# Kernel tuning notes

Measured on AMD Instinct MI355X. Metric: run time of the kernel, lower is better.

Reference implementation:

```python
import jax, jax.numpy as jnp
import numpy as np

N_NODES = 100000
N_EDGES = 1600000
D_IN, D_HID, D_OUT = 64, 64, 40


def _init_linear(key, out_c, in_c, bias=True):
    # PyTorch nn.Linear default init: U(-1/sqrt(in), 1/sqrt(in))
    bound = 1.0 / np.sqrt(in_c)
    kw, kb = jax.random.split(key)
    W = jax.random.uniform(kw, (out_c, in_c), jnp.float32, -bound, bound)
    if bias:
        b = jax.random.uniform(kb, (out_c,), jnp.float32, -bound, bound)
        return W, b
    return W


def setup_inputs() -> dict:
    key = jax.random.key(0)
    ks = jax.random.split(key, 8)
    x = jax.random.normal(ks[0], (N_NODES, D_IN), jnp.float32)
    edge_index = jax.random.randint(ks[1], (2, N_EDGES), 0, N_NODES, jnp.int64)
    W1l, b1 = _init_linear(ks[2], D_HID, D_IN, bias=True)   # lin_l (aggregated msgs)
    W1r = _init_linear(ks[3], D_HID, D_IN, bias=False)      # lin_r (root/self)
    W2l, b2 = _init_linear(ks[4], D_OUT, D_HID, bias=True)
    W2r = _init_linear(ks[5], D_OUT, D_HID, bias=False)
    return {"x": x, "edge_index": edge_index,
            "W1l": W1l, "b1": b1, "W1r": W1r,
            "W2l": W2l, "b2": b2, "W2r": W2r}


def _sage_conv(x, src, dst, Wl, bl, Wr):
    # mean aggregation of source-node features onto destination nodes
    msgs = x[src]                                            # [E, d] gather
    agg = jax.ops.segment_sum(msgs, dst, num_segments=N_NODES)
    deg = jax.ops.segment_sum(jnp.ones((src.shape[0],), x.dtype), dst,
                              num_segments=N_NODES)
    mean = agg / jnp.maximum(deg, 1.0)[:, None]              # [N, d]
    # out = lin_l(mean) + lin_r(x)
    return mean @ Wl.T + bl + x @ Wr.T


def reference(x, edge_index, W1l, b1, W1r, W2l, b2, W2r):
    src, dst = edge_index[0], edge_index[1]
    h = _sage_conv(x, src, dst, W1l, b1, W1r)
    h = jax.nn.relu(h)
    # dropout is identity in inference mode
    h = _sage_conv(h, src, dst, W2l, b2, W2r)
    return jax.nn.log_softmax(h, axis=1)
```

## Files before the change

kernel.cpp:

```cpp
#include <hip/hip_runtime.h>
#include <math.h>

#define N_NODES 100000
#define N_EDGES 1600000
#define D 64
#define DOUT 40
#define NBUCK ((N_NODES + 255) / 256)
#define CHUNK 4096
#define NCHUNK ((N_EDGES + CHUNK - 1) / CHUNK)
#define PTHREADS 512
#define BCAP 4864

typedef __attribute__((ext_vector_type(8))) short bf16x8v;
typedef __attribute__((ext_vector_type(4))) float f32x4v;

__device__ inline float bf2f(unsigned u) {
  union { unsigned i; float f; } v;
  v.i = u << 16;
  return v.f;
}
__device__ inline unsigned f2bf(float f) {
  union { float f; unsigned i; } v;
  v.f = f;
  unsigned r = v.i + 0x7fffu + ((v.i >> 16) & 1u);
  return r >> 16;
}
__device__ inline void addpk(float2& a, unsigned u) {
  union { unsigned i; float f; } lo, hi;
  lo.i = u << 16;
  hi.i = u & 0xffff0000u;
  a.x += lo.f;
  a.y += hi.f;
}
__device__ inline void addrow4(float2* A, uint4 r) {
  addpk(A[0], r.x); addpk(A[1], r.y); addpk(A[2], r.z); addpk(A[3], r.w);
}

__global__ __launch_bounds__(PTHREADS) void prep_kernel(
    const float* __restrict__ x, unsigned short* __restrict__ xbf,
    const float* __restrict__ W1l, const float* __restrict__ W1r,
    const float* __restrict__ W2l, const float* __restrict__ W2r,
    const float* __restrict__ b2, unsigned short* __restrict__ Wcat1,
    unsigned short* __restrict__ Wcat2, float* __restrict__ b2p,
    const int* __restrict__ src, const int* __restrict__ dst,
    int* __restrict__ bcnt, unsigned* __restrict__ binned) {
  __shared__ unsigned ent[CHUNK];
  __shared__ unsigned short sbk[CHUNK];
  __shared__ int cnt[512], scn[512], pos[512], base[512];
  int t = threadIdx.x;
  int blk = blockIdx.x;
  int gtid = blk * PTHREADS + t;
  int nth = NCHUNK * PTHREADS;

  const int n8 = N_NODES * D / 8;
  for (int i = gtid; i < n8; i += nth) {
    const float4* p = reinterpret_cast<const float4*>(x) + (size_t)i * 2;
    float4 a = p[0], b = p[1];
    uint4 o;
    o.x = f2bf(a.x) | (f2bf(a.y) << 16);
    o.y = f2bf(a.z) | (f2bf(a.w) << 16);
    o.z = f2bf(b.x) | (f2bf(b.y) << 16);
    o.w = f2bf(b.z) | (f2bf(b.w) << 16);
    reinterpret_cast<uint4*>(xbf)[i] = o;
  }
  const int NW = 64 * 128 + 48 * 128 + 48;
  for (int i = gtid; i < NW; i += nth) {
    if (i < 64 * 128) {
      int o = i >> 7, k = i & 127;
      float v = (k < 64) ? W1l[o * 64 + k] : W1r[o * 64 + (k - 64)];
      Wcat1[i] = (unsigned short)f2bf(v);
    } else if (i < 64 * 128 + 48 * 128) {
      int j = i - 64 * 128;
      int o = j >> 7, k = j & 127;
      float v = (o < DOUT) ? ((k < 64) ? W2l[o * 64 + k] : W2r[o * 64 + (k - 64)]) : 0.0f;
      Wcat2[j] = (unsigned short)f2bf(v);
    } else {
      int j = i - 64 * 128 - 48 * 128;
      b2p[j] = (j < DOUT) ? b2[j] : 0.0f;
    }
  }
  cnt[t] = 0;
  __syncthreads();
  int cbase = blk * CHUNK;
  int cc = min(CHUNK, N_EDGES - cbase);
  unsigned my_e[8];
  int my_b[8];
  int nmine = 0;
#pragma unroll
  for (int i = 0; i < 8; ++i) {
    int li = t + i * PTHREADS;
    if (li < cc) {
      int s = src[cbase + li];
      int d = dst[cbase + li];
      int b = d >> 8;
      my_e[nmine] = ((unsigned)(d & 255) << 24) | (unsigned)s;
      my_b[nmine] = b;
      nmine++;
      atomicAdd(&cnt[b], 1);
    }
  }
  __syncthreads();
  scn[t] = cnt[t];
  __syncthreads();
  for (int off = 1; off < 512; off <<= 1) {
    int v = (t >= off) ? scn[t - off] : 0;
    __syncthreads();
    scn[t] += v;
    __syncthreads();
  }
  pos[t] = scn[t] - cnt[t];
  __syncthreads();
  for (int i = 0; i < nmine; ++i) {
    int slot = atomicAdd(&pos[my_b[i]], 1);
    ent[slot] = my_e[i];
    sbk[slot] = (unsigned short)my_b[i];
  }
  __syncthreads();
  for (int b = t; b < NBUCK; b += PTHREADS)
    if (cnt[b] > 0) base[b] = atomicAdd(&bcnt[b], cnt[b]);
  __syncthreads();
  for (int i = t; i < cc; i += PTHREADS) {
    int b = sbk[i];
    int excl = scn[b] - cnt[b];
    binned[(size_t)b * BCAP + base[b] + (i - excl)] = ent[i];
  }
}

__global__ __launch_bounds__(512) void fine_kernel(
    const unsigned* __restrict__ binned, const int* __restrict__ bcnt,
    int* __restrict__ rs, int* __restrict__ re_, int* __restrict__ csr, int N) {
  __shared__ unsigned ent[BCAP];
  __shared__ int c[256], p[256], pos[256];
  int b = blockIdx.x;
  int t = threadIdx.x;
  int cc = bcnt[b];
  int s0 = b * BCAP;
  if (t < 256) c[t] = 0;
  __syncthreads();
  for (int i = t; i < cc; i += 512) {
    unsigned u = binned[s0 + i];
    ent[i] = u;
    atomicAdd(&c[u >> 24], 1);
  }
  __syncthreads();
  if (t < 256) p[t] = c[t];
  __syncthreads();
  for (int off = 1; off < 256; off <<= 1) {
    int v = 0;
    if (t < 256 && t >= off) v = p[t - off];
    __syncthreads();
    if (t < 256) p[t] += v;
    __syncthreads();
  }
  if (t < 256) {
    int excl = p[t] - c[t];
    int node = b * 256 + t;
    if (node < N) {
      rs[node] = s0 + excl;
      re_[node] = s0 + excl + c[t];
    }
    pos[t] = excl;
  }
  __syncthreads();
  for (int i = t; i < cc; i += 512) {
    unsigned u = ent[i];
    int slot = atomicAdd(&pos[u >> 24], 1);
    csr[s0 + slot] = (int)(u & 0xFFFFFFu);
  }
}

__global__ __launch_bounds__(256) void agg_kernel(
    const unsigned short* __restrict__ feat, const int* __restrict__ rs,
    const int* __restrict__ re_, const int* __restrict__ csr,
    unsigned short* __restrict__ msbf, int N) {
  int wv = (blockIdx.x * 256 + threadIdx.x) >> 6;
  int n0 = wv * 2;
  if (n0 >= N) return;
  int n1 = n0 + 1;
  int lane = threadIdx.x & 63;
  int g = lane >> 3;
  int t = lane & 7;
  int s0 = rs[n0], en0 = re_[n0];
  int s1 = rs[n1], en1 = re_[n1];
  float2 A[4] = {{0.f,0.f},{0.f,0.f},{0.f,0.f},{0.f,0.f}};
  float2 B[4] = {{0.f,0.f},{0.f,0.f},{0.f,0.f},{0.f,0.f}};
  int e0 = s0 + g, e1 = s1 + g;

  {
    bool v0a = e0 < en0, v0b = e0 + 8 < en0;
    bool v1a = e1 < en1, v1b = e1 + 8 < en1;
    int q0a = min(e0, max(en0 - 1, 0));
    int q0b = min(e0 + 8, max(en0 - 1, 0));
    int q1a = min(e1, max(en1 - 1, 0));
    int q1b = min(e1 + 8, max(en1 - 1, 0));
    int i0a = min(csr[q0a], N - 1);
    int i0b = min(csr[q0b], N - 1);
    int i1a = min(csr[q1a], N - 1);
    int i1b = min(csr[q1b], N - 1);
    uint4 r0a = *reinterpret_cast<const uint4*>(feat + (size_t)i0a * D + t * 8);
    uint4 r0b = *reinterpret_cast<const uint4*>(feat + (size_t)i0b * D + t * 8);
    uint4 r1a = *reinterpret_cast<const uint4*>(feat + (size_t)i1a * D + t * 8);
    uint4 r1b = *reinterpret_cast<const uint4*>(feat + (size_t)i1b * D + t * 8);
    if (v0a) addrow4(A, r0a);
    if (v0b) addrow4(A, r0b);
    if (v1a) addrow4(B, r1a);
    if (v1b) addrow4(B, r1b);
    e0 += 16;
    e1 += 16;
  }
  for (; e0 + 8 < en0; e0 += 16) {
    int i0 = csr[e0];
    int i1 = csr[e0 + 8];
    uint4 r0 = *reinterpret_cast<const uint4*>(feat + (size_t)i0 * D + t * 8);
    uint4 r1 = *reinterpret_cast<const uint4*>(feat + (size_t)i1 * D + t * 8);
    addrow4(A, r0);
    addrow4(A, r1);
  }
  if (e0 < en0) {
    int i0 = csr[e0];
    uint4 r0 = *reinterpret_cast<const uint4*>(feat + (size_t)i0 * D + t * 8);
    addrow4(A, r0);
  }
  for (; e1 + 8 < en1; e1 += 16) {
    int i0 = csr[e1];
    int i1 = csr[e1 + 8];
    uint4 r0 = *reinterpret_cast<const uint4*>(feat + (size_t)i0 * D + t * 8);
    uint4 r1 = *reinterpret_cast<const uint4*>(feat + (size_t)i1 * D + t * 8);
    addrow4(B, r0);
    addrow4(B, r1);
  }
  if (e1 < en1) {
    int i0 = csr[e1];
    uint4 r0 = *reinterpret_cast<const uint4*>(feat + (size_t)i0 * D + t * 8);
    addrow4(B, r0);
  }
#pragma unroll
  for (int j = 0; j < 4; ++j) {
    A[j].x += __shfl_xor(A[j].x, 8, 64);  A[j].y += __shfl_xor(A[j].y, 8, 64);
    A[j].x += __shfl_xor(A[j].x, 16, 64); A[j].y += __shfl_xor(A[j].y, 16, 64);
    A[j].x += __shfl_xor(A[j].x, 32, 64); A[j].y += __shfl_xor(A[j].y, 32, 64);
    B[j].x += __shfl_xor(B[j].x, 8, 64);  B[j].y += __shfl_xor(B[j].y, 8, 64);
    B[j].x += __shfl_xor(B[j].x, 16, 64); B[j].y += __shfl_xor(B[j].y, 16, 64);
    B[j].x += __shfl_xor(B[j].x, 32, 64); B[j].y += __shfl_xor(B[j].y, 32, 64);
  }
  float inv0 = 1.0f / fmaxf((float)(en0 - s0), 1.0f);
  float inv1 = 1.0f / fmaxf((float)(en1 - s1), 1.0f);
  float va[8] = {A[0].x, A[0].y, A[1].x, A[1].y, A[2].x, A[2].y, A[3].x, A[3].y};
  float vb[8] = {B[0].x, B[0].y, B[1].x, B[1].y, B[2].x, B[2].y, B[3].x, B[3].y};
  float ma = va[0], mb = vb[0];
#pragma unroll
  for (int j = 1; j < 8; ++j) {
    if (g == j) { ma = va[j]; mb = vb[j]; }
  }
  msbf[(size_t)n0 * D + t * 8 + g] = (unsigned short)f2bf(ma * inv0);
  msbf[(size_t)n1 * D + t * 8 + g] = (unsigned short)f2bf(mb * inv1);
}

__global__ __launch_bounds__(256) void lin1_kernel(
    const unsigned short* __restrict__ xbf, const unsigned short* __restrict__ msbf,
    const unsigned short* __restrict__ Wcat, const float* __restrict__ b1,
    unsigned short* __restrict__ hbf, int N) {
  int wid = (blockIdx.x * 256 + threadIdx.x) >> 6;
  int ntiles = N >> 4;
  if (wid >= ntiles) return;
  int lane = threadIdx.x & 63;
  int col = lane & 15;
  int k0 = (lane >> 4) * 8;
  int base = wid * 16;
  const unsigned short* am = msbf + (size_t)(base + col) * D;
  const unsigned short* ax = xbf + (size_t)(base + col) * D;
  bf16x8v a0 = *(const bf16x8v*)(am + k0);
  bf16x8v a1 = *(const bf16x8v*)(am + 32 + k0);
  bf16x8v a2 = *(const bf16x8v*)(ax + k0);
  bf16x8v a3 = *(const bf16x8v*)(ax + 32 + k0);
  f32x4v acc0 = {0.f, 0.f, 0.f, 0.f}, acc1 = acc0, acc2 = acc0, acc3 = acc0;
#define LIN1_CT(CT, ACC)                                                      \
  {                                                                           \
    const unsigned short* w = Wcat + ((CT)*16 + col) * 128 + k0;              \
    bf16x8v b0 = *(const bf16x8v*)(w);                                        \
    bf16x8v b1v = *(const bf16x8v*)(w + 32);                                  \
    bf16x8v b2v = *(const bf16x8v*)(w + 64);                                  \
    bf16x8v b3v = *(const bf16x8v*)(w + 96);                                  \
    ACC = __builtin_amdgcn_mfma_f32_16x16x32_bf16(a0, b0, ACC, 0, 0, 0);      \
    ACC = __builtin_amdgcn_mfma_f32_16x16x32_bf16(a1, b1v, ACC, 0, 0, 0);     \
    ACC = __builtin_amdgcn_mfma_f32_16x16x32_bf16(a2, b2v, ACC, 0, 0, 0);     \
    ACC = __builtin_amdgcn_mfma_f32_16x16x32_bf16(a3, b3v, ACC, 0, 0, 0);     \
  }
  LIN1_CT(0, acc0) LIN1_CT(1, acc1) LIN1_CT(2, acc2) LIN1_CT(3, acc3)
#undef LIN1_CT
  int rbase = (lane >> 4) * 4;
  float bias0 = b1[col], bias1 = b1[16 + col], bias2 = b1[32 + col], bias3 = b1[48 + col];
#pragma unroll
  for (int r = 0; r < 4; ++r) {
    size_t rowoff = (size_t)(base + rbase + r) * D;
    hbf[rowoff + col]      = (unsigned short)f2bf(fmaxf(acc0[r] + bias0, 0.f));
    hbf[rowoff + 16 + col] = (unsigned short)f2bf(fmaxf(acc1[r] + bias1, 0.f));
    hbf[rowoff + 32 + col] = (unsigned short)f2bf(fmaxf(acc2[r] + bias2, 0.f));
    hbf[rowoff + 48 + col] = (unsigned short)f2bf(fmaxf(acc3[r] + bias3, 0.f));
  }
}

__global__ __launch_bounds__(256) void lin2_kernel(
    const unsigned short* __restrict__ hbf, const unsigned short* __restrict__ msbf,
    const unsigned short* __restrict__ Wcat, const float* __restrict__ b2p,
    float* __restrict__ out, int N) {
  int wid = (blockIdx.x * 256 + threadIdx.x) >> 6;
  int ntiles = N >> 4;
  if (wid >= ntiles) return;
  int lane = threadIdx.x & 63;
  int col = lane & 15;
  int k0 = (lane >> 4) * 8;
  int base = wid * 16;
  const unsigned short* am = msbf + (size_t)(base + col) * D;
  const unsigned short* ah = hbf + (size_t)(base + col) * D;
  bf16x8v a0 = *(const bf16x8v*)(am + k0);
  bf16x8v a1 = *(const bf16x8v*)(am + 32 + k0);
  bf16x8v a2 = *(const bf16x8v*)(ah + k0);
  bf16x8v a3 = *(const bf16x8v*)(ah + 32 + k0);
  f32x4v acc0 = {0.f, 0.f, 0.f, 0.f}, acc1 = acc0, acc2 = acc0;
#define LIN2_CT(CT, ACC)                                                      \
  {                                                                           \
    const unsigned short* w = Wcat + ((CT)*16 + col) * 128 + k0;              \
    bf16x8v b0 = *(const bf16x8v*)(w);                                        \
    bf16x8v b1v = *(const bf16x8v*)(w + 32);                                  \
    bf16x8v b2v = *(const bf16x8v*)(w + 64);                                  \
    bf16x8v b3v = *(const bf16x8v*)(w + 96);                                  \
    ACC = __builtin_amdgcn_mfma_f32_16x16x32_bf16(a0, b0, ACC, 0, 0, 0);      \
    ACC = __builtin_amdgcn_mfma_f32_16x16x32_bf16(a1, b1v, ACC, 0, 0, 0);     \
    ACC = __builtin_amdgcn_mfma_f32_16x16x32_bf16(a2, b2v, ACC, 0, 0, 0);     \
    ACC = __builtin_amdgcn_mfma_f32_16x16x32_bf16(a3, b3v, ACC, 0, 0, 0);     \
  }
  LIN2_CT(0, acc0) LIN2_CT(1, acc1) LIN2_CT(2, acc2)
#undef LIN2_CT
  int rbase = (lane >> 4) * 4;
  float bias0 = b2p[col], bias1 = b2p[16 + col], bias2 = b2p[32 + col];
  bool v2ok = (col < 8);
#pragma unroll
  for (int r = 0; r < 4; ++r) {
    float v0 = acc0[r] + bias0;
    float v1 = acc1[r] + bias1;
    float v2 = v2ok ? (acc2[r] + bias2) : -INFINITY;
    float mx = fmaxf(fmaxf(v0, v1), v2);
    mx = fmaxf(mx, __shfl_xor(mx, 1, 64));
    mx = fmaxf(mx, __shfl_xor(mx, 2, 64));
    mx = fmaxf(mx, __shfl_xor(mx, 4, 64));
    mx = fmaxf(mx, __shfl_xor(mx, 8, 64));
    float sm = expf(v0 - mx) + expf(v1 - mx) + (v2ok ? expf(v2 - mx) : 0.f);
    sm += __shfl_xor(sm, 1, 64);
    sm += __shfl_xor(sm, 2, 64);
    sm += __shfl_xor(sm, 4, 64);
    sm += __shfl_xor(sm, 8, 64);
    float ls = mx + logf(sm);
    size_t rowoff = (size_t)(base + rbase + r) * DOUT;
    out[rowoff + col] = v0 - ls;
    out[rowoff + 16 + col] = v1 - ls;
    if (v2ok) out[rowoff + 32 + col] = v2 - ls;
  }
}

extern "C" void kernel_launch(void* const* d_in, const int* in_sizes, int n_in,
                              void* d_out, int out_size, void* d_ws, size_t ws_size,
                              hipStream_t stream) {
  const float* x   = (const float*)d_in[0];
  const int*   ei  = (const int*)d_in[1];
  const float* W1l = (const float*)d_in[2];
  const float* b1  = (const float*)d_in[3];
  const float* W1r = (const float*)d_in[4];
  const float* W2l = (const float*)d_in[5];
  const float* b2  = (const float*)d_in[6];
  const float* W2r = (const float*)d_in[7];
  float* out = (float*)d_out;

  const int* src = ei;
  const int* dst = ei + N_EDGES;

  char* ws = (char*)d_ws;
  size_t featB = (size_t)N_NODES * D * sizeof(unsigned short);
  unsigned short* xbf = (unsigned short*)ws;
  unsigned short* hbf = (unsigned short*)(ws + featB);
  int* csr  = (int*)(ws + 2 * featB);
  int* rs   = csr + (size_t)NBUCK * BCAP;
  int* re_  = rs + N_NODES;
  int* bcnt = re_ + N_NODES;
  char* scratch = (char*)(bcnt + NBUCK);
  scratch = (char*)(((uintptr_t)scratch + 15) & ~(uintptr_t)15);
  unsigned* binned     = (unsigned*)scratch;
  unsigned short* ms1  = (unsigned short*)scratch;
  unsigned short* ms2  = xbf;
  unsigned short* Wcat1 = (unsigned short*)(scratch + featB);
  unsigned short* Wcat2 = Wcat1 + 64 * 128;
  float* b2p            = (float*)(Wcat2 + 48 * 128);

  const int AGG_BLOCKS = (N_NODES + 7) / 8;
  const int LIN_BLOCKS = ((N_NODES / 16) + 3) / 4;

  hipMemsetAsync(bcnt, 0, NBUCK * sizeof(int), stream);
  prep_kernel<<<NCHUNK, PTHREADS, 0, stream>>>(x, xbf, W1l, W1r, W2l, W2r, b2,
                                               Wcat1, Wcat2, b2p, src, dst, bcnt, binned);
  fine_kernel<<<NBUCK, 512, 0, stream>>>(binned, bcnt, rs, re_, csr, N_NODES);

  agg_kernel<<<AGG_BLOCKS, 256, 0, stream>>>(xbf, rs, re_, csr, ms1, N_NODES);
  lin1_kernel<<<LIN_BLOCKS, 256, 0, stream>>>(xbf, ms1, Wcat1, b1, hbf, N_NODES);

  agg_kernel<<<AGG_BLOCKS, 256, 0, stream>>>(hbf, rs, re_, csr, ms2, N_NODES);
  lin2_kernel<<<LIN_BLOCKS, 256, 0, stream>>>(hbf, ms2, Wcat2, b2p, out, N_NODES);
}
```

Baseline: 147.1 us.

## Fuse neighbor aggregation with linear layers via shared-memory tiles

Merges the agg and lin kernels of each SAGE layer into one kernel. Each 512-thread block aggregates 16 nodes, eight waves doing two nodes each, and writes the bf16 means into LDS. After a barrier, one wave runs the MFMA linear layer and the epilogue. This removes the global round-trip for the mean features and two kernel launches. In exchange, seven of eight waves sit idle during the matmul phase, and the block-level barrier ties the MFMA work to the slowest gather wave.

```diff
diff --git a/kernel.cpp b/kernel.cpp
--- a/kernel.cpp
+++ b/kernel.cpp
@@ -169,23 +169,16 @@
   }
 }
 
-__global__ __launch_bounds__(256) void agg_kernel(
-    const unsigned short* __restrict__ feat, const int* __restrict__ rs,
-    const int* __restrict__ re_, const int* __restrict__ csr,
-    unsigned short* __restrict__ msbf, int N) {
-  int wv = (blockIdx.x * 256 + threadIdx.x) >> 6;
-  int n0 = wv * 2;
-  if (n0 >= N) return;
+__device__ inline void agg2(const unsigned short* __restrict__ feat,
+                            const int* __restrict__ rs, const int* __restrict__ re_,
+                            const int* __restrict__ csr, int n0, int N,
+                            int g, int t, float& ma, float& mb) {
   int n1 = n0 + 1;
-  int lane = threadIdx.x & 63;
-  int g = lane >> 3;
-  int t = lane & 7;
   int s0 = rs[n0], en0 = re_[n0];
   int s1 = rs[n1], en1 = re_[n1];
   float2 A[4] = {{0.f,0.f},{0.f,0.f},{0.f,0.f},{0.f,0.f}};
   float2 B[4] = {{0.f,0.f},{0.f,0.f},{0.f,0.f},{0.f,0.f}};
   int e0 = s0 + g, e1 = s1 + g;
-
   {
     bool v0a = e0 < en0, v0b = e0 + 8 < en0;
     bool v1a = e1 < en1, v1b = e1 + 8 < en1;
@@ -247,114 +240,130 @@
   float inv1 = 1.0f / fmaxf((float)(en1 - s1), 1.0f);
   float va[8] = {A[0].x, A[0].y, A[1].x, A[1].y, A[2].x, A[2].y, A[3].x, A[3].y};
   float vb[8] = {B[0].x, B[0].y, B[1].x, B[1].y, B[2].x, B[2].y, B[3].x, B[3].y};
-  float ma = va[0], mb = vb[0];
+  ma = va[0]; mb = vb[0];
 #pragma unroll
   for (int j = 1; j < 8; ++j) {
     if (g == j) { ma = va[j]; mb = vb[j]; }
   }
-  msbf[(size_t)n0 * D + t * 8 + g] = (unsigned short)f2bf(ma * inv0);
-  msbf[(size_t)n1 * D + t * 8 + g] = (unsigned short)f2bf(mb * inv1);
-}
-
-__global__ __launch_bounds__(256) void lin1_kernel(
-    const unsigned short* __restrict__ xbf, const unsigned short* __restrict__ msbf,
+  ma *= inv0;
+  mb *= inv1;
+}
+
+__global__ __launch_bounds__(512) void fused1_kernel(
+    const unsigned short* __restrict__ xbf, const int* __restrict__ rs,
+    const int* __restrict__ re_, const int* __restrict__ csr,
     const unsigned short* __restrict__ Wcat, const float* __restrict__ b1,
     unsigned short* __restrict__ hbf, int N) {
-  int wid = (blockIdx.x * 256 + threadIdx.x) >> 6;
-  int ntiles = N >> 4;
-  if (wid >= ntiles) return;
+  __shared__ unsigned short msL[16][64];
+  int w = threadIdx.x >> 6;
   int lane = threadIdx.x & 63;
-  int col = lane & 15;
-  int k0 = (lane >> 4) * 8;
-  int base = wid * 16;
-  const unsigned short* am = msbf + (size_t)(base + col) * D;
-  const unsigned short* ax = xbf + (size_t)(base + col) * D;
-  bf16x8v a0 = *(const bf16x8v*)(am + k0);
-  bf16x8v a1 = *(const bf16x8v*)(am + 32 + k0);
-  bf16x8v a2 = *(const bf16x8v*)(ax + k0);
-  bf16x8v a3 = *(const bf16x8v*)(ax + 32 + k0);
-  f32x4v acc0 = {0.f, 0.f, 0.f, 0.f}, acc1 = acc0, acc2 = acc0, acc3 = acc0;
+  int g = lane >> 3;
+  int t = lane & 7;
+  int base = blockIdx.x * 16;
+  float ma, mb;
+  agg2(xbf, rs, re_, csr, base + w * 2, N, g, t, ma, mb);
+  msL[w * 2][t * 8 + g] = (unsigned short)f2bf(ma);
+  msL[w * 2 + 1][t * 8 + g] = (unsigned short)f2bf(mb);
+  __syncthreads();
+  if (threadIdx.x < 64) {
+    int col = lane & 15;
+    int k0 = (lane >> 4) * 8;
+    bf16x8v a0 = *(const bf16x8v*)(&msL[col][k0]);
+    bf16x8v a1 = *(const bf16x8v*)(&msL[col][32 + k0]);
+    const unsigned short* ax = xbf + (size_t)(base + col) * D;
+    bf16x8v a2 = *(const bf16x8v*)(ax + k0);
+    bf16x8v a3 = *(const bf16x8v*)(ax + 32 + k0);
+    f32x4v acc0 = {0.f, 0.f, 0.f, 0.f}, acc1 = acc0, acc2 = acc0, acc3 = acc0;
 #define LIN1_CT(CT, ACC)                                                      \
-  {                                                                           \
-    const unsigned short* w = Wcat + ((CT)*16 + col) * 128 + k0;              \
-    bf16x8v b0 = *(const bf16x8v*)(w);                                        \
-    bf16x8v b1v = *(const bf16x8v*)(w + 32);                                  \
-    bf16x8v b2v = *(const bf16x8v*)(w + 64);                                  \
-    bf16x8v b3v = *(const bf16x8v*)(w + 96);                                  \
-    ACC = __builtin_amdgcn_mfma_f32_16x16x32_bf16(a0, b0, ACC, 0, 0, 0);      \
-    ACC = __builtin_amdgcn_mfma_f32_16x16x32_bf16(a1, b1v, ACC, 0, 0, 0);     \
-    ACC = __builtin_amdgcn_mfma_f32_16x16x32_bf16(a2, b2v, ACC, 0, 0, 0);     \
-    ACC = __builtin_amdgcn_mfma_f32_16x16x32_bf16(a3, b3v, ACC, 0, 0, 0);     \
-  }
-  LIN1_CT(0, acc0) LIN1_CT(1, acc1) LIN1_CT(2, acc2) LIN1_CT(3, acc3)
+    {                                                                         \
+      const unsigned short* wp = Wcat + ((CT)*16 + col) * 128 + k0;           \
+      bf16x8v b0 = *(const bf16x8v*)(wp);                                     \
+      bf16x8v b1v = *(const bf16x8v*)(wp + 32);                               \
+      bf16x8v b2v = *(const bf16x8v*)(wp + 64);                               \
+      bf16x8v b3v = *(const bf16x8v*)(wp + 96);                               \
+      ACC = __builtin_amdgcn_mfma_f32_16x16x32_bf16(a0, b0, ACC, 0, 0, 0);    \
+      ACC = __builtin_amdgcn_mfma_f32_16x16x32_bf16(a1, b1v, ACC, 0, 0, 0);   \
+      ACC = __builtin_amdgcn_mfma_f32_16x16x32_bf16(a2, b2v, ACC, 0, 0, 0);   \
+      ACC = __builtin_amdgcn_mfma_f32_16x16x32_bf16(a3, b3v, ACC, 0, 0, 0);   \
+    }
+    LIN1_CT(0, acc0) LIN1_CT(1, acc1) LIN1_CT(2, acc2) LIN1_CT(3, acc3)
 #undef LIN1_CT
-  int rbase = (lane >> 4) * 4;
-  float bias0 = b1[col], bias1 = b1[16 + col], bias2 = b1[32 + col], bias3 = b1[48 + col];
+    int rbase = (lane >> 4) * 4;
+    float bias0 = b1[col], bias1 = b1[16 + col], bias2 = b1[32 + col], bias3 = b1[48 + col];
 #pragma unroll
-  for (int r = 0; r < 4; ++r) {
-    size_t rowoff = (size_t)(base + rbase + r) * D;
-    hbf[rowoff + col]      = (unsigned short)f2bf(fmaxf(acc0[r] + bias0, 0.f));
-    hbf[rowoff + 16 + col] = (unsigned short)f2bf(fmaxf(acc1[r] + bias1, 0.f));
-    hbf[rowoff + 32 + col] = (unsigned short)f2bf(fmaxf(acc2[r] + bias2, 0.f));
-    hbf[rowoff + 48 + col] = (unsigned short)f2bf(fmaxf(acc3[r] + bias3, 0.f));
-  }
-}
-
-__global__ __launch_bounds__(256) void lin2_kernel(
-    const unsigned short* __restrict__ hbf, const unsigned short* __restrict__ msbf,
+    for (int r = 0; r < 4; ++r) {
+      size_t rowoff = (size_t)(base + rbase + r) * D;
+      hbf[rowoff + col]      = (unsigned short)f2bf(fmaxf(acc0[r] + bias0, 0.f));
+      hbf[rowoff + 16 + col] = (unsigned short)f2bf(fmaxf(acc1[r] + bias1, 0.f));
+      hbf[rowoff + 32 + col] = (unsigned short)f2bf(fmaxf(acc2[r] + bias2, 0.f));
+      hbf[rowoff + 48 + col] = (unsigned short)f2bf(fmaxf(acc3[r] + bias3, 0.f));
+    }
+  }
+}
+
+__global__ __launch_bounds__(512) void fused2_kernel(
+    const unsigned short* __restrict__ hbf, const int* __restrict__ rs,
+    const int* __restrict__ re_, const int* __restrict__ csr,
     const unsigned short* __restrict__ Wcat, const float* __restrict__ b2p,
     float* __restrict__ out, int N) {
-  int wid = (blockIdx.x * 256 + threadIdx.x) >> 6;
-  int ntiles = N >> 4;
-  if (wid >= ntiles) return;
+  __shared__ unsigned short msL[16][64];
+  int w = threadIdx.x >> 6;
   int lane = threadIdx.x & 63;
-  int col = lane & 15;
-  int k0 = (lane >> 4) * 8;
-  int base = wid * 16;
-  const unsigned short* am = msbf + (size_t)(base + col) * D;
-  const unsigned short* ah = hbf + (size_t)(base + col) * D;
-  bf16x8v a0 = *(const bf16x8v*)(am + k0);
-  bf16x8v a1 = *(const bf16x8v*)(am + 32 + k0);
-  bf16x8v a2 = *(const bf16x8v*)(ah + k0);
-  bf16x8v a3 = *(const bf16x8v*)(ah + 32 + k0);
-  f32x4v acc0 = {0.f, 0.f, 0.f, 0.f}, acc1 = acc0, acc2 = acc0;
+  int g = lane >> 3;
+  int t = lane & 7;
+  int base = blockIdx.x * 16;
+  float ma, mb;
+  agg2(hbf, rs, re_, csr, base + w * 2, N, g, t, ma, mb);
+  msL[w * 2][t * 8 + g] = (unsigned short)f2bf(ma);
+  msL[w * 2 + 1][t * 8 + g] = (unsigned short)f2bf(mb);
+  __syncthreads();
+  if (threadIdx.x < 64) {
+    int col = lane & 15;
+    int k0 = (lane >> 4) * 8;
+    bf16x8v a0 = *(const bf16x8v*)(&msL[col][k0]);
+    bf16x8v a1 = *(const bf16x8v*)(&msL[col][32 + k0]);
+    const unsigned short* ah = hbf + (size_t)(base + col) * D;
+    bf16x8v a2 = *(const bf16x8v*)(ah + k0);
+    bf16x8v a3 = *(const bf16x8v*)(ah + 32 + k0);
+    f32x4v acc0 = {0.f, 0.f, 0.f, 0.f}, acc1 = acc0, acc2 = acc0;
 #define LIN2_CT(CT, ACC)                                                      \
-  {                                                                           \
-    const unsigned short* w = Wcat + ((CT)*16 + col) * 128 + k0;              \
-    bf16x8v b0 = *(const bf16x8v*)(w);                                        \
-    bf16x8v b1v = *(const bf16x8v*)(w + 32);                                  \
-    bf16x8v b2v = *(const bf16x8v*)(w + 64);                                  \
-    bf16x8v b3v = *(const bf16x8v*)(w + 96);                                  \
-    ACC = __builtin_amdgcn_mfma_f32_16x16x32_bf16(a0, b0, ACC, 0, 0, 0);      \
-    ACC = __builtin_amdgcn_mfma_f32_16x16x32_bf16(a1, b1v, ACC, 0, 0, 0);     \
-    ACC = __builtin_amdgcn_mfma_f32_16x16x32_bf16(a2, b2v, ACC, 0, 0, 0);     \
-    ACC = __builtin_amdgcn_mfma_f32_16x16x32_bf16(a3, b3v, ACC, 0, 0, 0);     \
-  }
-  LIN2_CT(0, acc0) LIN2_CT(1, acc1) LIN2_CT(2, acc2)
+    {                                                                         \
+      const unsigned short* wp = Wcat + ((CT)*16 + col) * 128 + k0;           \
+      bf16x8v b0 = *(const bf16x8v*)(wp);                                     \
+      bf16x8v b1v = *(const bf16x8v*)(wp + 32);                               \
+      bf16x8v b2v = *(const bf16x8v*)(wp + 64);                               \
+      bf16x8v b3v = *(const bf16x8v*)(wp + 96);                               \
+      ACC = __builtin_amdgcn_mfma_f32_16x16x32_bf16(a0, b0, ACC, 0, 0, 0);    \
+      ACC = __builtin_amdgcn_mfma_f32_16x16x32_bf16(a1, b1v, ACC, 0, 0, 0);   \
+      ACC = __builtin_amdgcn_mfma_f32_16x16x32_bf16(a2, b2v, ACC, 0, 0, 0);   \
+      ACC = __builtin_amdgcn_mfma_f32_16x16x32_bf16(a3, b3v, ACC, 0, 0, 0);   \
+    }
+    LIN2_CT(0, acc0) LIN2_CT(1, acc1) LIN2_CT(2, acc2)
 #undef LIN2_CT
-  int rbase = (lane >> 4) * 4;
-  float bias0 = b2p[col], bias1 = b2p[16 + col], bias2 = b2p[32 + col];
-  bool v2ok = (col < 8);
+    int rbase = (lane >> 4) * 4;
+    float bias0 = b2p[col], bias1 = b2p[16 + col], bias2 = b2p[32 + col];
+    bool v2ok = (col < 8);
 #pragma unroll
-  for (int r = 0; r < 4; ++r) {
-    float v0 = acc0[r] + bias0;
-    float v1 = acc1[r] + bias1;
-    float v2 = v2ok ? (acc2[r] + bias2) : -INFINITY;
-    float mx = fmaxf(fmaxf(v0, v1), v2);
-    mx = fmaxf(mx, __shfl_xor(mx, 1, 64));
-    mx = fmaxf(mx, __shfl_xor(mx, 2, 64));
-    mx = fmaxf(mx, __shfl_xor(mx, 4, 64));
-    mx = fmaxf(mx, __shfl_xor(mx, 8, 64));
-    float sm = expf(v0 - mx) + expf(v1 - mx) + (v2ok ? expf(v2 - mx) : 0.f);
-    sm += __shfl_xor(sm, 1, 64);
-    sm += __shfl_xor(sm, 2, 64);
-    sm += __shfl_xor(sm, 4, 64);
-    sm += __shfl_xor(sm, 8, 64);
-    float ls = mx + logf(sm);
-    size_t rowoff = (size_t)(base + rbase + r) * DOUT;
-    out[rowoff + col] = v0 - ls;
-    out[rowoff + 16 + col] = v1 - ls;
-    if (v2ok) out[rowoff + 32 + col] = v2 - ls;
+    for (int r = 0; r < 4; ++r) {
+      float v0 = acc0[r] + bias0;
+      float v1 = acc1[r] + bias1;
+      float v2 = v2ok ? (acc2[r] + bias2) : -INFINITY;
+      float mx = fmaxf(fmaxf(v0, v1), v2);
+      mx = fmaxf(mx, __shfl_xor(mx, 1, 64));
+      mx = fmaxf(mx, __shfl_xor(mx, 2, 64));
+      mx = fmaxf(mx, __shfl_xor(mx, 4, 64));
+      mx = fmaxf(mx, __shfl_xor(mx, 8, 64));
+      float sm = expf(v0 - mx) + expf(v1 - mx) + (v2ok ? expf(v2 - mx) : 0.f);
+      sm += __shfl_xor(sm, 1, 64);
+      sm += __shfl_xor(sm, 2, 64);
+      sm += __shfl_xor(sm, 4, 64);
+      sm += __shfl_xor(sm, 8, 64);
+      float ls = mx + logf(sm);
+      size_t rowoff = (size_t)(base + rbase + r) * DOUT;
+      out[rowoff + col] = v0 - ls;
+      out[rowoff + 16 + col] = v1 - ls;
+      if (v2ok) out[rowoff + 32 + col] = v2 - ls;
+    }
   }
 }
 
@@ -384,24 +393,18 @@
   int* bcnt = re_ + N_NODES;
   char* scratch = (char*)(bcnt + NBUCK);
   scratch = (char*)(((uintptr_t)scratch + 15) & ~(uintptr_t)15);
-  unsigned* binned     = (unsigned*)scratch;
-  unsigned short* ms1  = (unsigned short*)scratch;
-  unsigned short* ms2  = xbf;
-  unsigned short* Wcat1 = (unsigned short*)(scratch + featB);
+  unsigned* binned      = (unsigned*)scratch;
+  unsigned short* Wcat1 = (unsigned short*)(scratch + (size_t)NBUCK * BCAP * 4);
   unsigned short* Wcat2 = Wcat1 + 64 * 128;
   float* b2p            = (float*)(Wcat2 + 48 * 128);
 
-  const int AGG_BLOCKS = (N_NODES + 7) / 8;
-  const int LIN_BLOCKS = ((N_NODES / 16) + 3) / 4;
+  const int NTILES = N_NODES / 16;
 
   hipMemsetAsync(bcnt, 0, NBUCK * sizeof(int), stream);
   prep_kernel<<<NCHUNK, PTHREADS, 0, stream>>>(x, xbf, W1l, W1r, W2l, W2r, b2,
                                                Wcat1, Wcat2, b2p, src, dst, bcnt, binned);
   fine_kernel<<<NBUCK, 512, 0, stream>>>(binned, bcnt, rs, re_, csr, N_NODES);
 
-  agg_kernel<<<AGG_BLOCKS, 256, 0, stream>>>(xbf, rs, re_, csr, ms1, N_NODES);
-  lin1_kernel<<<LIN_BLOCKS, 256, 0, stream>>>(xbf, ms1, Wcat1, b1, hbf, N_NODES);
-
-  agg_kernel<<<AGG_BLOCKS, 256, 0, stream>>>(hbf, rs, re_, csr, ms2, N_NODES);
-  lin2_kernel<<<LIN_BLOCKS, 256, 0, stream>>>(hbf, ms2, Wcat2, b2p, out, N_NODES);
-}
+  fused1_kernel<<<NTILES, 512, 0, stream>>>(xbf, rs, re_, csr, Wcat1, b1, hbf, N_NODES);
+  fused2_kernel<<<NTILES, 512, 0, stream>>>(hbf, rs, re_, csr, Wcat2, b2p, out, N_NODES);
+}
```

Measured after the change: 141.6 us. 1.04x faster.
